# Optimization experiments

Hardware: AMD Instinct MI355X
Metric: run time of the kernel (lower is better)

The kernel has to match this reference:

```python
import jax, jax.numpy as jnp
import numpy as np

N_HEADS = 16

def setup_inputs() -> dict:
    key = jax.random.key(0)
    ks = jax.random.split(key, 6)
    B, S, D = 2, 2048, 1024
    return {
        "hidden_states": jax.random.normal(ks[0], (B, S, D), dtype=jnp.float32),
        "Wq": jax.random.normal(ks[1], (D, D), dtype=jnp.float32) * (1.0 / np.sqrt(D)),
        "Wk": jax.random.normal(ks[2], (D, D), dtype=jnp.float32) * (1.0 / np.sqrt(D)),
        "Wv": jax.random.normal(ks[3], (D, D), dtype=jnp.float32) * (1.0 / np.sqrt(D)),
        "Wo": jax.random.normal(ks[4], (D, D), dtype=jnp.float32) * (1.0 / np.sqrt(D)),
        "bo": jnp.zeros((D,), dtype=jnp.float32),
    }

def reference(hidden_states, Wq, Wk, Wv, Wo, bo):
    B, S, D = hidden_states.shape
    H = N_HEADS
    hd = D // H  # head_dim; d_kv == d_model per module's final view
    # nn.Linear(bias=False): x @ W.T, then the module's direct view to (B, H, S, hd)
    q = (hidden_states @ Wq.T).reshape(B, H, S, hd)
    k = (hidden_states @ Wk.T).reshape(B, H, S, hd)  # self-attention path (encoder_states=None)
    v = (hidden_states @ Wv.T).reshape(B, H, S, hd)
    # naive full score matrix [B, H, S, S]
    wei = jnp.einsum('bhqd,bhkd->bhqk', q, k)
    causal = jnp.tril(jnp.ones((S, S), dtype=bool))
    wei = jnp.where(causal, wei, -jnp.inf)
    # NOTE: module divides logits by head_dim (not sqrt) -- preserved faithfully
    attn = jax.nn.softmax(wei / hd, axis=-1)
    ctx = jnp.einsum('bhqk,bhkd->bhqd', attn, v)  # [B, H, S, hd]
    out = ctx.transpose(0, 2, 1, 3).reshape(B, S, D)
    return out @ Wo.T + bo
```

## Files before the change

kernel.cpp:

```cpp
#include <hip/hip_runtime.h>

#define S_LEN   2048
#define D_MODEL 1024
#define N_HEADS 16
#define HEAD_DIM 64

typedef unsigned short u16;
typedef float  floatx4 __attribute__((ext_vector_type(4)));
typedef short  bf16x8  __attribute__((ext_vector_type(8)));

__device__ __forceinline__ u16 f2bf(float f) {
    unsigned int u = __float_as_uint(f);
    u += 0x7FFF + ((u >> 16) & 1);
    return (u16)(u >> 16);
}
__device__ __forceinline__ unsigned pack2bf(float a, float b) {
    return (unsigned)f2bf(a) | ((unsigned)f2bf(b) << 16);
}

__device__ __forceinline__ void gload_lds16(const void* g, void* l) {
    __builtin_amdgcn_global_load_lds(
        reinterpret_cast<const __attribute__((address_space(1))) unsigned int*>(
            reinterpret_cast<uintptr_t>(g)),
        reinterpret_cast<__attribute__((address_space(3))) unsigned int*>(
            reinterpret_cast<uintptr_t>(l)),
        16, 0, 0);
}

__global__ __launch_bounds__(256) void cast_all(const float* __restrict__ hs,
                                                const float* __restrict__ w0,
                                                const float* __restrict__ w1,
                                                const float* __restrict__ w2,
                                                const float* __restrict__ w3,
                                                u16* __restrict__ dst) {
    const size_t NHS = (size_t)2 * S_LEN * D_MODEL;
    const size_t e0 = (size_t)blockIdx.x * 2048;
    const float* src;
    size_t base;
    if (e0 < NHS)                 { src = hs; base = 0; }
    else {
        const int wi = (int)((e0 - NHS) >> 20);
        src = wi == 0 ? w0 : wi == 1 ? w1 : wi == 2 ? w2 : w3;
        base = NHS + ((size_t)wi << 20);
    }
    const size_t i = e0 + (size_t)threadIdx.x * 8;
    const float4 a = *(const float4*)(src + (i - base));
    const float4 b = *(const float4*)(src + (i - base) + 4);
    uint4 o;
    o.x = pack2bf(a.x, a.y); o.y = pack2bf(a.z, a.w);
    o.z = pack2bf(b.x, b.y); o.w = pack2bf(b.z, b.w);
    *(uint4*)(dst + i) = o;
}

__global__ __launch_bounds__(256) void vtrans(const u16* __restrict__ Vf,
                                              u16* __restrict__ Vt) {
    __shared__ unsigned T[64 * 133];
    const int bh = blockIdx.y;
    const int sBase = blockIdx.x * 128;
    const u16* src = Vf + (size_t)bh * (S_LEN * HEAD_DIM) + (size_t)sBase * HEAD_DIM;
    u16* dst = Vt + (size_t)bh * (S_LEN * HEAD_DIM) + sBase;
    const int tid = threadIdx.x;

#pragma unroll
    for (int it = 0; it < 4; ++it) {
        const int idx = it * 256 + tid;
        const int row = idx >> 3, ch = idx & 7;
        const float4 v4 = *(const float4*)(src + row * 64 + ch * 8);
        const u16* vs = (const u16*)&v4;
#pragma unroll
        for (int j = 0; j < 8; ++j) T[(ch * 8 + j) * 133 + row] = vs[j];
    }
    __syncthreads();
#pragma unroll
    for (int it = 0; it < 4; ++it) {
        const int idx = it * 256 + tid;
        const int d = idx >> 4, sc = idx & 15;
        union { u16 u[8]; float4 f; } tmp;
#pragma unroll
        for (int j = 0; j < 8; ++j) tmp.u[j] = (u16)T[d * 133 + sc * 8 + j];
        *(float4*)(dst + (size_t)d * S_LEN + sc * 8) = tmp.f;
    }
}

__global__ __launch_bounds__(256) void gemm_qkv(const u16* __restrict__ A,
                                                const u16* __restrict__ Wq,
                                                const u16* __restrict__ Wk,
                                                const u16* __restrict__ Wv,
                                                u16* __restrict__ Qo,
                                                u16* __restrict__ Ko,
                                                u16* __restrict__ Vfo) {
    __shared__ u16 As[8 * 512];
    __shared__ u16 Ws[8 * 512];

    const int blk = blockIdx.x;
    const int y   = (blk & 7) | (((blk >> 3) & 3) << 3);
    const int x   = blk >> 5;
    const int which = x >> 3;
    const int nBase = (x & 7) * 128;
    const int mBase = y * 128;
    const u16* W = which == 0 ? Wq : which == 1 ? Wk : Wv;

    const int tid = threadIdx.x, lane = tid & 63, wv = tid >> 6;
    const int l15 = lane & 15, quad = lane >> 4;
    const int wm = wv & 1, wn = wv >> 1;
    const int srow = lane >> 2;
    const int gch  = (lane & 3) ^ ((lane >> 3) & 3);
    const int swz  = (l15 >> 1) & 3;

    floatx4 acc[4][4];
#pragma unroll
    for (int i = 0; i < 4; ++i)
#pragma unroll
        for (int j = 0; j < 4; ++j) acc[i][j] = (floatx4)(0.0f);

    for (int k0 = 0; k0 < D_MODEL; k0 += 32) {
        __syncthreads();
#pragma unroll
        for (int t = 0; t < 2; ++t) {
            const int ci = wv * 2 + t;
            gload_lds16(A + (size_t)(mBase + ci * 16 + srow) * D_MODEL + k0 + gch * 8,
                        &As[ci * 512]);
            gload_lds16(W + (size_t)(nBase + ci * 16 + srow) * D_MODEL + k0 + gch * 8,
                        &Ws[ci * 512]);
        }
        __syncthreads();

        bf16x8 af[4], bfr[4];
#pragma unroll
        for (int mt = 0; mt < 4; ++mt)
            af[mt] = *(const bf16x8*)&As[(wm * 64 + mt * 16 + l15) * 32 + (quad ^ swz) * 8];
#pragma unroll
        for (int nt = 0; nt < 4; ++nt)
            bfr[nt] = *(const bf16x8*)&Ws[(wn * 64 + nt * 16 + l15) * 32 + (quad ^ swz) * 8];
#pragma unroll
        for (int mt = 0; mt < 4; ++mt)
#pragma unroll
            for (int nt = 0; nt < 4; ++nt)
                acc[mt][nt] = __builtin_amdgcn_mfma_f32_16x16x32_bf16(af[mt], bfr[nt], acc[mt][nt], 0, 0, 0);
    }

    u16* O = which == 0 ? Qo : (which == 1 ? Ko : Vfo);
    const float scale = which == 0 ? (1.44269504088896f / 64.0f) : 1.0f;
#pragma unroll
    for (int mt = 0; mt < 4; ++mt)
#pragma unroll
        for (int nt = 0; nt < 4; ++nt) {
            const int col = nBase + wn * 64 + nt * 16 + l15;
#pragma unroll
            for (int r = 0; r < 4; ++r) {
                const int row = mBase + wm * 64 + mt * 16 + quad * 4 + r;
                O[(size_t)row * D_MODEL + col] = f2bf(acc[mt][nt][r] * scale);
            }
        }
}

__global__ __launch_bounds__(256) void gemm_out(const u16* __restrict__ A,
                                                const u16* __restrict__ W,
                                                const float* __restrict__ bias,
                                                float* __restrict__ C) {
    __shared__ u16 As[4 * 512];
    __shared__ u16 Ws[8 * 512];

    const int nBase = blockIdx.x * 128;
    const int mBase = blockIdx.y * 64;
    const int tid = threadIdx.x, lane = tid & 63, wv = tid >> 6;
    const int l15 = lane & 15, quad = lane >> 4;
    const int wm = wv & 1, wn = wv >> 1;
    const int srow = lane >> 2;
    const int gch  = (lane & 3) ^ ((lane >> 3) & 3);
    const int swz  = (l15 >> 1) & 3;

    floatx4 acc[2][4];
#pragma unroll
    for (int i = 0; i < 2; ++i)
#pragma unroll
        for (int j = 0; j < 4; ++j) acc[i][j] = (floatx4)(0.0f);

    for (int k0 = 0; k0 < D_MODEL; k0 += 32) {
        __syncthreads();
        gload_lds16(A + (size_t)(mBase + wv * 16 + srow) * D_MODEL + k0 + gch * 8,
                    &As[wv * 512]);
#pragma unroll
        for (int t = 0; t < 2; ++t) {
            const int ci = wv * 2 + t;
            gload_lds16(W + (size_t)(nBase + ci * 16 + srow) * D_MODEL + k0 + gch * 8,
                        &Ws[ci * 512]);
        }
        __syncthreads();

        bf16x8 af[2], bfr[4];
#pragma unroll
        for (int mt = 0; mt < 2; ++mt)
            af[mt] = *(const bf16x8*)&As[(wm * 32 + mt * 16 + l15) * 32 + (quad ^ swz) * 8];
#pragma unroll
        for (int nt = 0; nt < 4; ++nt)
            bfr[nt] = *(const bf16x8*)&Ws[(wn * 64 + nt * 16 + l15) * 32 + (quad ^ swz) * 8];
#pragma unroll
        for (int mt = 0; mt < 2; ++mt)
#pragma unroll
            for (int nt = 0; nt < 4; ++nt)
                acc[mt][nt] = __builtin_amdgcn_mfma_f32_16x16x32_bf16(af[mt], bfr[nt], acc[mt][nt], 0, 0, 0);
    }

#pragma unroll
    for (int mt = 0; mt < 2; ++mt)
#pragma unroll
        for (int nt = 0; nt < 4; ++nt) {
            const int col = nBase + wn * 64 + nt * 16 + l15;
            const float bv = bias[col];
#pragma unroll
            for (int r = 0; r < 4; ++r) {
                const int row = mBase + wm * 32 + mt * 16 + quad * 4 + r;
                C[(size_t)row * D_MODEL + col] = acc[mt][nt][r] + bv;
            }
        }
}

__global__ __launch_bounds__(256) void attn4(const u16* __restrict__ Q,
                                             const u16* __restrict__ K,
                                             const u16* __restrict__ Vt,
                                             u16* __restrict__ Ctx) {
    __shared__ u16 Ks[8 * 512];
    __shared__ u16 Vs[8 * 512];
    __shared__ u16 Ps[4][16 * 72];

    const int flat = blockIdx.x;
    const int g    = flat & 31;
    const int qt   = 31 - (flat >> 5);
    const int h = g & 15, b = g >> 4;

    const int tid = threadIdx.x, lane = tid & 63, wv = tid >> 6;
    const int l15 = lane & 15, quad = lane >> 4;

    const size_t headOff = ((size_t)b * N_HEADS + h) * S_LEN * HEAD_DIM;
    const u16* Qh = Q + headOff;
    const u16* Kh = K + headOff;
    const u16* Vh = Vt + headOff;
    u16* Cb = Ctx + (size_t)b * S_LEN * D_MODEL + (size_t)h * HEAD_DIM;

    const int srow = lane >> 3;
    const int gch  = (lane & 7) ^ srow;
    const int swz  = l15 & 7;

    const int qBase = qt * 64;

    bf16x8 qa[2];
#pragma unroll
    for (int ks = 0; ks < 2; ++ks)
        qa[ks] = *(const bf16x8*)(Qh + (size_t)(qBase + wv * 16 + l15) * 64 + ks * 32 + quad * 8);

    floatx4 o[4];
#pragma unroll
    for (int nt = 0; nt < 4; ++nt) o[nt] = (floatx4)(0.0f);
    float lp = 0.0f;

    for (int kt = 0; kt <= qt; ++kt) {
        const int kBase = kt * 64;
        __syncthreads();
#pragma unroll
        for (int t = 0; t < 2; ++t) {
            const int ci = wv * 2 + t;
            gload_lds16(Kh + (size_t)(kBase + ci * 8 + srow) * 64 + gch * 8, &Ks[ci * 512]);
            gload_lds16(Vh + (size_t)(ci * 8 + srow) * S_LEN + kBase + gch * 8, &Vs[ci * 512]);
        }
        __syncthreads();

        floatx4 s[4];
#pragma unroll
        for (int mt = 0; mt < 4; ++mt) {
            s[mt] = (floatx4)(0.0f);
#pragma unroll
            for (int ks = 0; ks < 2; ++ks) {
                const bf16x8 kb = *(const bf16x8*)&Ks[(mt * 16 + l15) * 64 + ((ks * 4 + quad) ^ swz) * 8];
                s[mt] = __builtin_amdgcn_mfma_f32_16x16x32_bf16(kb, qa[ks], s[mt], 0, 0, 0);
            }
        }

        const bool diag = (kt == qt);
#pragma unroll
        for (int mt = 0; mt < 4; ++mt) {
            float p[4];
#pragma unroll
            for (int r = 0; r < 4; ++r) {
                float pv = exp2f(s[mt][r]);
                if (diag && (mt * 16 + quad * 4 + r > wv * 16 + l15)) pv = 0.0f;
                p[r] = pv;
                lp += pv;
            }
            uint2 w;
            w.x = __builtin_amdgcn_perm(__float_as_uint(p[1]), __float_as_uint(p[0]), 0x07060302);
            w.y = __builtin_amdgcn_perm(__float_as_uint(p[3]), __float_as_uint(p[2]), 0x07060302);
            *(uint2*)&Ps[wv][l15 * 72 + mt * 16 + quad * 4] = w;
        }

        bf16x8 pa[2];
#pragma unroll
        for (int ks = 0; ks < 2; ++ks)
            pa[ks] = *(const bf16x8*)&Ps[wv][l15 * 72 + ks * 32 + quad * 8];
#pragma unroll
        for (int nt = 0; nt < 4; ++nt)
#pragma unroll
            for (int ks = 0; ks < 2; ++ks) {
                const bf16x8 vb = *(const bf16x8*)&Vs[(nt * 16 + l15) * 64 + ((ks * 4 + quad) ^ swz) * 8];
                o[nt] = __builtin_amdgcn_mfma_f32_16x16x32_bf16(pa[ks], vb, o[nt], 0, 0, 0);
            }
    }

    lp += __shfl_xor(lp, 16);
    lp += __shfl_xor(lp, 32);

#pragma unroll
    for (int r = 0; r < 4; ++r) {
        const float inv = 1.0f / __shfl(lp, quad * 4 + r);
        const int row = qBase + wv * 16 + quad * 4 + r;
#pragma unroll
        for (int nt = 0; nt < 4; ++nt)
            Cb[(size_t)row * D_MODEL + nt * 16 + l15] = f2bf(o[nt][r] * inv);
    }
}

extern "C" void kernel_launch(void* const* d_in, const int* in_sizes, int n_in,
                              void* d_out, int out_size, void* d_ws, size_t ws_size,
                              hipStream_t stream) {
    const float* hs = (const float*)d_in[0];
    const float* Wq = (const float*)d_in[1];
    const float* Wk = (const float*)d_in[2];
    const float* Wv = (const float*)d_in[3];
    const float* Wo = (const float*)d_in[4];
    const float* bo = (const float*)d_in[5];
    float* out = (float*)d_out;

    const size_t NHS = (size_t)2 * S_LEN * D_MODEL;
    const size_t NW  = (size_t)D_MODEL * D_MODEL;

    u16* hsb = (u16*)d_ws;
    u16* Wb  = hsb + NHS;
    u16* Qb  = Wb + 4 * NW;
    u16* Kb  = Qb + NHS;
    u16* Vfb = Kb + NHS;
    u16* Vtb = Vfb + NHS;
    u16* Cxb = Vtb + NHS;

    cast_all<<<4096, 256, 0, stream>>>(hs, Wq, Wk, Wv, Wo, hsb);

    gemm_qkv<<<768, 256, 0, stream>>>(hsb, Wb, Wb + NW, Wb + 2 * NW,
                                      Qb, Kb, Vfb);

    vtrans<<<dim3(16, 32), 256, 0, stream>>>(Vfb, Vtb);

    attn4<<<1024, 256, 0, stream>>>(Qb, Kb, Vtb, Cxb);

    gemm_out<<<dim3(8, 64), 256, 0, stream>>>(Cxb, Wb + 3 * NW, bo, out);
}
```

Before: 181.4 us.

## Process two query tiles per attention block to reuse loaded K/V tiles

The attention kernel now assigns 128 query rows (two 64-row sub-tiles) to each block instead of 64, so each K/V tile staged into shared memory feeds both sub-tiles. This halves the global K/V loads and the barriers per query row, and the grid shrinks from 1024 to 512 blocks. In exchange each thread holds twice the accumulators, which raises register pressure, and fewer blocks may reduce occupancy and load balance across CUs.

```diff
diff --git a/kernel.cpp b/kernel.cpp
--- a/kernel.cpp
+++ b/kernel.cpp
@@ -216,7 +216,51 @@
         }
 }
 
-__global__ __launch_bounds__(256) void attn4(const u16* __restrict__ Q,
+__device__ __forceinline__ void attn_sub(const u16* __restrict__ Ks,
+                                         const u16* __restrict__ Vs,
+                                         u16* __restrict__ Psw,
+                                         const bf16x8 qa[2],
+                                         floatx4 o[4], float& lp,
+                                         bool diag, int l15, int quad, int wv, int swz) {
+    floatx4 s[4];
+#pragma unroll
+    for (int mt = 0; mt < 4; ++mt) {
+        s[mt] = (floatx4)(0.0f);
+#pragma unroll
+        for (int ks = 0; ks < 2; ++ks) {
+            const bf16x8 kb = *(const bf16x8*)&Ks[(mt * 16 + l15) * 64 + ((ks * 4 + quad) ^ swz) * 8];
+            s[mt] = __builtin_amdgcn_mfma_f32_16x16x32_bf16(kb, qa[ks], s[mt], 0, 0, 0);
+        }
+    }
+#pragma unroll
+    for (int mt = 0; mt < 4; ++mt) {
+        float p[4];
+#pragma unroll
+        for (int r = 0; r < 4; ++r) {
+            float pv = exp2f(s[mt][r]);
+            if (diag && (mt * 16 + quad * 4 + r > wv * 16 + l15)) pv = 0.0f;
+            p[r] = pv;
+            lp += pv;
+        }
+        uint2 w;
+        w.x = __builtin_amdgcn_perm(__float_as_uint(p[1]), __float_as_uint(p[0]), 0x07060302);
+        w.y = __builtin_amdgcn_perm(__float_as_uint(p[3]), __float_as_uint(p[2]), 0x07060302);
+        *(uint2*)&Psw[l15 * 72 + mt * 16 + quad * 4] = w;
+    }
+    bf16x8 pa[2];
+#pragma unroll
+    for (int ks = 0; ks < 2; ++ks)
+        pa[ks] = *(const bf16x8*)&Psw[l15 * 72 + ks * 32 + quad * 8];
+#pragma unroll
+    for (int nt = 0; nt < 4; ++nt)
+#pragma unroll
+        for (int ks = 0; ks < 2; ++ks) {
+            const bf16x8 vb = *(const bf16x8*)&Vs[(nt * 16 + l15) * 64 + ((ks * 4 + quad) ^ swz) * 8];
+            o[nt] = __builtin_amdgcn_mfma_f32_16x16x32_bf16(pa[ks], vb, o[nt], 0, 0, 0);
+        }
+}
+
+__global__ __launch_bounds__(256) void attn5(const u16* __restrict__ Q,
                                              const u16* __restrict__ K,
                                              const u16* __restrict__ Vt,
                                              u16* __restrict__ Ctx) {
@@ -226,7 +270,7 @@
 
     const int flat = blockIdx.x;
     const int g    = flat & 31;
-    const int qt   = 31 - (flat >> 5);
+    const int qb   = 15 - (flat >> 5);
     const int h = g & 15, b = g >> 4;
 
     const int tid = threadIdx.x, lane = tid & 63, wv = tid >> 6;
@@ -242,19 +286,23 @@
     const int gch  = (lane & 7) ^ srow;
     const int swz  = l15 & 7;
 
-    const int qBase = qt * 64;
-
-    bf16x8 qa[2];
-#pragma unroll
-    for (int ks = 0; ks < 2; ++ks)
-        qa[ks] = *(const bf16x8*)(Qh + (size_t)(qBase + wv * 16 + l15) * 64 + ks * 32 + quad * 8);
-
-    floatx4 o[4];
-#pragma unroll
-    for (int nt = 0; nt < 4; ++nt) o[nt] = (floatx4)(0.0f);
-    float lp = 0.0f;
-
-    for (int kt = 0; kt <= qt; ++kt) {
+    const int qBase = qb * 128;
+
+    bf16x8 qa[2][2];
+#pragma unroll
+    for (int sub = 0; sub < 2; ++sub)
+#pragma unroll
+        for (int ks = 0; ks < 2; ++ks)
+            qa[sub][ks] = *(const bf16x8*)(Qh + (size_t)(qBase + sub * 64 + wv * 16 + l15) * 64
+                                           + ks * 32 + quad * 8);
+
+    floatx4 oA[4], oB[4];
+#pragma unroll
+    for (int nt = 0; nt < 4; ++nt) { oA[nt] = (floatx4)(0.0f); oB[nt] = (floatx4)(0.0f); }
+    float lpA = 0.0f, lpB = 0.0f;
+
+    const int kmax = 2 * qb + 1;
+    for (int kt = 0; kt <= kmax; ++kt) {
         const int kBase = kt * 64;
         __syncthreads();
 #pragma unroll
@@ -265,57 +313,24 @@
         }
         __syncthreads();
 
-        floatx4 s[4];
-#pragma unroll
-        for (int mt = 0; mt < 4; ++mt) {
-            s[mt] = (floatx4)(0.0f);
-#pragma unroll
-            for (int ks = 0; ks < 2; ++ks) {
-                const bf16x8 kb = *(const bf16x8*)&Ks[(mt * 16 + l15) * 64 + ((ks * 4 + quad) ^ swz) * 8];
-                s[mt] = __builtin_amdgcn_mfma_f32_16x16x32_bf16(kb, qa[ks], s[mt], 0, 0, 0);
-            }
-        }
-
-        const bool diag = (kt == qt);
-#pragma unroll
-        for (int mt = 0; mt < 4; ++mt) {
-            float p[4];
-#pragma unroll
-            for (int r = 0; r < 4; ++r) {
-                float pv = exp2f(s[mt][r]);
-                if (diag && (mt * 16 + quad * 4 + r > wv * 16 + l15)) pv = 0.0f;
-                p[r] = pv;
-                lp += pv;
-            }
-            uint2 w;
-            w.x = __builtin_amdgcn_perm(__float_as_uint(p[1]), __float_as_uint(p[0]), 0x07060302);
-            w.y = __builtin_amdgcn_perm(__float_as_uint(p[3]), __float_as_uint(p[2]), 0x07060302);
-            *(uint2*)&Ps[wv][l15 * 72 + mt * 16 + quad * 4] = w;
-        }
-
-        bf16x8 pa[2];
-#pragma unroll
-        for (int ks = 0; ks < 2; ++ks)
-            pa[ks] = *(const bf16x8*)&Ps[wv][l15 * 72 + ks * 32 + quad * 8];
-#pragma unroll
-        for (int nt = 0; nt < 4; ++nt)
-#pragma unroll
-            for (int ks = 0; ks < 2; ++ks) {
-                const bf16x8 vb = *(const bf16x8*)&Vs[(nt * 16 + l15) * 64 + ((ks * 4 + quad) ^ swz) * 8];
-                o[nt] = __builtin_amdgcn_mfma_f32_16x16x32_bf16(pa[ks], vb, o[nt], 0, 0, 0);
-            }
-    }
-
-    lp += __shfl_xor(lp, 16);
-    lp += __shfl_xor(lp, 32);
+        if (kt <= 2 * qb)
+            attn_sub(Ks, Vs, Ps[wv], qa[0], oA, lpA, kt == 2 * qb, l15, quad, wv, swz);
+        attn_sub(Ks, Vs, Ps[wv], qa[1], oB, lpB, kt == kmax, l15, quad, wv, swz);
+    }
+
+    lpA += __shfl_xor(lpA, 16); lpA += __shfl_xor(lpA, 32);
+    lpB += __shfl_xor(lpB, 16); lpB += __shfl_xor(lpB, 32);
 
 #pragma unroll
     for (int r = 0; r < 4; ++r) {
-        const float inv = 1.0f / __shfl(lp, quad * 4 + r);
-        const int row = qBase + wv * 16 + quad * 4 + r;
-#pragma unroll
-        for (int nt = 0; nt < 4; ++nt)
-            Cb[(size_t)row * D_MODEL + nt * 16 + l15] = f2bf(o[nt][r] * inv);
+        const float invA = 1.0f / __shfl(lpA, quad * 4 + r);
+        const float invB = 1.0f / __shfl(lpB, quad * 4 + r);
+        const int rowA = qBase + wv * 16 + quad * 4 + r;
+#pragma unroll
+        for (int nt = 0; nt < 4; ++nt) {
+            Cb[(size_t)rowA * D_MODEL + nt * 16 + l15]        = f2bf(oA[nt][r] * invA);
+            Cb[(size_t)(rowA + 64) * D_MODEL + nt * 16 + l15] = f2bf(oB[nt][r] * invB);
+        }
     }
 }
 
@@ -348,7 +363,7 @@
 
     vtrans<<<dim3(16, 32), 256, 0, stream>>>(Vfb, Vtb);
 
-    attn4<<<1024, 256, 0, stream>>>(Qb, Kb, Vtb, Cxb);
+    attn5<<<512, 256, 0, stream>>>(Qb, Kb, Vtb, Cxb);
 
     gemm_out<<<dim3(8, 64), 256, 0, stream>>>(Cxb, Wb + 3 * NW, bo, out);
 }
```

Result: slower. 195.3 us (+7.7%).

## Split attention across key slices per wave and reduce partial outputs via LDS

Applied to the files above, without the earlier changes.

The attention kernel now gives each wave a 16-key slice of every key tile instead of 16 query rows. Each wave computes scores for all 64 queries and keeps P in registers, feeding it directly into 16x16x16 MFMAs. This removes the per-tile LDS round trip for P. The partial O accumulators and row sums from the four waves are then combined through LDS at the end. The cost is more accumulator registers (occupancy hint of 3), a multi-step cross-wave reduction epilogue with extra syncs and about 35KB of LDS, and skipped work for fully masked diagonal groups.

```diff
diff --git a/kernel.cpp b/kernel.cpp
--- a/kernel.cpp
+++ b/kernel.cpp
@@ -8,6 +8,7 @@
 typedef unsigned short u16;
 typedef float  floatx4 __attribute__((ext_vector_type(4)));
 typedef short  bf16x8  __attribute__((ext_vector_type(8)));
+typedef short  bf16x4  __attribute__((ext_vector_type(4)));
 
 __device__ __forceinline__ u16 f2bf(float f) {
     unsigned int u = __float_as_uint(f);
@@ -216,13 +217,15 @@
         }
 }
 
-__global__ __launch_bounds__(256) void attn4(const u16* __restrict__ Q,
-                                             const u16* __restrict__ K,
-                                             const u16* __restrict__ Vt,
-                                             u16* __restrict__ Ctx) {
-    __shared__ u16 Ks[8 * 512];
-    __shared__ u16 Vs[8 * 512];
-    __shared__ u16 Ps[4][16 * 72];
+__global__ __launch_bounds__(256, 3) void attn6(const u16* __restrict__ Q,
+                                                const u16* __restrict__ K,
+                                                const u16* __restrict__ Vt,
+                                                u16* __restrict__ Ctx) {
+    __shared__ u16 Ks[4096];
+    __shared__ u16 Vs[4096];
+    __shared__ float RedA[64 * 68];
+    __shared__ float RedB[64 * 68];
+    __shared__ float lpbuf[4 * 64];
 
     const int flat = blockIdx.x;
     const int g    = flat & 31;
@@ -244,15 +247,20 @@
 
     const int qBase = qt * 64;
 
-    bf16x8 qa[2];
-#pragma unroll
-    for (int ks = 0; ks < 2; ++ks)
-        qa[ks] = *(const bf16x8*)(Qh + (size_t)(qBase + wv * 16 + l15) * 64 + ks * 32 + quad * 8);
-
-    floatx4 o[4];
-#pragma unroll
-    for (int nt = 0; nt < 4; ++nt) o[nt] = (floatx4)(0.0f);
-    float lp = 0.0f;
+    bf16x8 qb[4][2];
+#pragma unroll
+    for (int qg = 0; qg < 4; ++qg)
+#pragma unroll
+        for (int ks = 0; ks < 2; ++ks)
+            qb[qg][ks] = *(const bf16x8*)(Qh + (size_t)(qBase + qg * 16 + l15) * 64
+                                          + ks * 32 + quad * 8);
+
+    floatx4 o[4][4];
+#pragma unroll
+    for (int qg = 0; qg < 4; ++qg)
+#pragma unroll
+        for (int dg = 0; dg < 4; ++dg) o[qg][dg] = (floatx4)(0.0f);
+    float lp[4] = {0.0f, 0.0f, 0.0f, 0.0f};
 
     for (int kt = 0; kt <= qt; ++kt) {
         const int kBase = kt * 64;
@@ -265,57 +273,99 @@
         }
         __syncthreads();
 
+        bf16x8 ka[2];
+#pragma unroll
+        for (int ks = 0; ks < 2; ++ks)
+            ka[ks] = *(const bf16x8*)&Ks[(wv * 16 + l15) * 64 + ((ks * 4 + quad) ^ swz) * 8];
+
+        bf16x4 vb[4];
+#pragma unroll
+        for (int dg = 0; dg < 4; ++dg)
+            vb[dg] = *(const bf16x4*)&Vs[(dg * 16 + l15) * 64
+                                         + (((wv * 2 + (quad >> 1)) ^ swz) * 8) + (quad & 1) * 4];
+
         floatx4 s[4];
 #pragma unroll
-        for (int mt = 0; mt < 4; ++mt) {
-            s[mt] = (floatx4)(0.0f);
-#pragma unroll
-            for (int ks = 0; ks < 2; ++ks) {
-                const bf16x8 kb = *(const bf16x8*)&Ks[(mt * 16 + l15) * 64 + ((ks * 4 + quad) ^ swz) * 8];
-                s[mt] = __builtin_amdgcn_mfma_f32_16x16x32_bf16(kb, qa[ks], s[mt], 0, 0, 0);
+        for (int qg = 0; qg < 4; ++qg) {
+            s[qg] = (floatx4)(0.0f);
+#pragma unroll
+            for (int ks = 0; ks < 2; ++ks)
+                s[qg] = __builtin_amdgcn_mfma_f32_16x16x32_bf16(ka[ks], qb[qg][ks], s[qg], 0, 0, 0);
+        }
+
+        const bool diag = (kt == qt);
+#pragma unroll
+        for (int qg = 0; qg < 4; ++qg) {
+            if (diag && qg < wv) continue;
+            float p[4];
+#pragma unroll
+            for (int r = 0; r < 4; ++r) {
+                float pv = __builtin_amdgcn_exp2f(s[qg][r]);
+                if (diag && qg == wv && (quad * 4 + r > l15)) pv = 0.0f;
+                p[r] = pv;
+                lp[qg] += pv;
             }
-        }
-
-        const bool diag = (kt == qt);
-#pragma unroll
-        for (int mt = 0; mt < 4; ++mt) {
-            float p[4];
+            union { uint2 u; bf16x4 v; } pk;
+            pk.u.x = __builtin_amdgcn_perm(__float_as_uint(p[1]), __float_as_uint(p[0]), 0x07060302);
+            pk.u.y = __builtin_amdgcn_perm(__float_as_uint(p[3]), __float_as_uint(p[2]), 0x07060302);
+#pragma unroll
+            for (int dg = 0; dg < 4; ++dg)
+                o[qg][dg] = __builtin_amdgcn_mfma_f32_16x16x16bf16_1k(pk.v, vb[dg], o[qg][dg], 0, 0, 0);
+        }
+    }
+
+#pragma unroll
+    for (int qg = 0; qg < 4; ++qg) {
+        lp[qg] += __shfl_xor(lp[qg], 16);
+        lp[qg] += __shfl_xor(lp[qg], 32);
+    }
+    lpbuf[wv * 64 + quad * 16 + l15] = lp[quad];
+
+    if (wv == 1 || wv == 3) {
+        float* R = (wv == 1) ? RedA : RedB;
+#pragma unroll
+        for (int qg = 0; qg < 4; ++qg)
+#pragma unroll
+            for (int dg = 0; dg < 4; ++dg)
+                *(floatx4*)&R[(dg * 16 + l15) * 68 + qg * 16 + quad * 4] = o[qg][dg];
+    }
+    __syncthreads();
+    if (wv == 0 || wv == 2) {
+        const float* R = (wv == 0) ? RedA : RedB;
+#pragma unroll
+        for (int qg = 0; qg < 4; ++qg)
+#pragma unroll
+            for (int dg = 0; dg < 4; ++dg)
+                o[qg][dg] += *(const floatx4*)&R[(dg * 16 + l15) * 68 + qg * 16 + quad * 4];
+    }
+    __syncthreads();
+    if (wv == 2) {
+#pragma unroll
+        for (int qg = 0; qg < 4; ++qg)
+#pragma unroll
+            for (int dg = 0; dg < 4; ++dg)
+                *(floatx4*)&RedA[(dg * 16 + l15) * 68 + qg * 16 + quad * 4] = o[qg][dg];
+    }
+    __syncthreads();
+    if (wv == 0) {
+#pragma unroll
+        for (int qg = 0; qg < 4; ++qg) {
+#pragma unroll
+            for (int dg = 0; dg < 4; ++dg)
+                o[qg][dg] += *(const floatx4*)&RedA[(dg * 16 + l15) * 68 + qg * 16 + quad * 4];
+            floatx4 lt = *(const floatx4*)&lpbuf[0 * 64 + qg * 16 + quad * 4];
+            lt += *(const floatx4*)&lpbuf[1 * 64 + qg * 16 + quad * 4];
+            lt += *(const floatx4*)&lpbuf[2 * 64 + qg * 16 + quad * 4];
+            lt += *(const floatx4*)&lpbuf[3 * 64 + qg * 16 + quad * 4];
 #pragma unroll
             for (int r = 0; r < 4; ++r) {
-                float pv = exp2f(s[mt][r]);
-                if (diag && (mt * 16 + quad * 4 + r > wv * 16 + l15)) pv = 0.0f;
-                p[r] = pv;
-                lp += pv;
+                const float inv = 1.0f / lt[r];
+                const int row = qBase + qg * 16 + quad * 4 + r;
+#pragma unroll
+                for (int dg = 0; dg < 4; ++dg)
+                    Cb[(size_t)row * D_MODEL + dg * 16 + l15] = f2bf(o[qg][dg][r] * inv);
             }
-            uint2 w;
-            w.x = __builtin_amdgcn_perm(__float_as_uint(p[1]), __float_as_uint(p[0]), 0x07060302);
-            w.y = __builtin_amdgcn_perm(__float_as_uint(p[3]), __float_as_uint(p[2]), 0x07060302);
-            *(uint2*)&Ps[wv][l15 * 72 + mt * 16 + quad * 4] = w;
-        }
-
-        bf16x8 pa[2];
-#pragma unroll
-        for (int ks = 0; ks < 2; ++ks)
-            pa[ks] = *(const bf16x8*)&Ps[wv][l15 * 72 + ks * 32 + quad * 8];
-#pragma unroll
-        for (int nt = 0; nt < 4; ++nt)
-#pragma unroll
-            for (int ks = 0; ks < 2; ++ks) {
-                const bf16x8 vb = *(const bf16x8*)&Vs[(nt * 16 + l15) * 64 + ((ks * 4 + quad) ^ swz) * 8];
-                o[nt] = __builtin_amdgcn_mfma_f32_16x16x32_bf16(pa[ks], vb, o[nt], 0, 0, 0);
-            }
-    }
-
-    lp += __shfl_xor(lp, 16);
-    lp += __shfl_xor(lp, 32);
-
-#pragma unroll
-    for (int r = 0; r < 4; ++r) {
-        const float inv = 1.0f / __shfl(lp, quad * 4 + r);
-        const int row = qBase + wv * 16 + quad * 4 + r;
-#pragma unroll
-        for (int nt = 0; nt < 4; ++nt)
-            Cb[(size_t)row * D_MODEL + nt * 16 + l15] = f2bf(o[nt][r] * inv);
+        }
     }
 }
 
@@ -348,7 +398,7 @@
 
     vtrans<<<dim3(16, 32), 256, 0, stream>>>(Vfb, Vtb);
 
-    attn4<<<1024, 256, 0, stream>>>(Qb, Kb, Vtb, Cxb);
+    attn6<<<1024, 256, 0, stream>>>(Qb, Kb, Vtb, Cxb);
 
     gemm_out<<<dim3(8, 64), 256, 0, stream>>>(Cxb, Wb + 3 * NW, bo, out);
 }
```

New measurement: 172.7 us. -4.8%, faster.
